# Optimization experiments

Hardware: AMD Instinct MI355X
Metric: run time of the kernel (lower is better)

Reference implementation:

```python
import jax, jax.numpy as jnp
import numpy as np
from jax import lax


def _bilinear_gather(img, ys, xs):
    """img: [B,H,W,C]; ys,xs: [B,K,H,W] fractional coords. Zero padding outside.
    Returns [B,K,H,W,C]."""
    B, H, W, C = img.shape
    y0 = jnp.floor(ys)
    x0 = jnp.floor(xs)
    wy = (ys - y0)[..., None]
    wx = (xs - x0)[..., None]
    y0i = y0.astype(jnp.int32)
    x0i = x0.astype(jnp.int32)
    flat = img.reshape(B, H * W, C)

    def gather(yi, xi):
        valid = (yi >= 0) & (yi < H) & (xi >= 0) & (xi < W)
        yc = jnp.clip(yi, 0, H - 1)
        xc = jnp.clip(xi, 0, W - 1)
        idx = (yc * W + xc).reshape(B, -1, 1)
        g = jnp.take_along_axis(flat, idx, axis=1).reshape(yi.shape + (C,))
        return g * valid[..., None].astype(img.dtype)

    v00 = gather(y0i, x0i)
    v01 = gather(y0i, x0i + 1)
    v10 = gather(y0i + 1, x0i)
    v11 = gather(y0i + 1, x0i + 1)
    one = jnp.asarray(1.0, img.dtype)
    return (v00 * (one - wy) * (one - wx) + v01 * (one - wy) * wx
            + v10 * wy * (one - wx) + v11 * wy * wx)


def _forward(x, w_off, b_off, w_def, b_def, w_attn, b_attn):
    B, Cin, H, W = x.shape
    Cout = w_def.shape[0]
    # offset conv: 3x3, pad 1 -> [B, 18, H, W]
    off = lax.conv_general_dilated(x, w_off, (1, 1), ((1, 1), (1, 1)))
    off = off + b_off[None, :, None, None]
    off = off.reshape(B, 9, 2, H, W)
    dy = off[:, :, 0]  # [B,9,H,W], torchvision order: (dy, dx) per kernel pt
    dx = off[:, :, 1]
    # kernel point grid, row-major over (kh, kw)
    ky, kx = jnp.meshgrid(jnp.arange(3), jnp.arange(3), indexing='ij')
    ky = ky.reshape(9).astype(x.dtype)
    kx = kx.reshape(9).astype(x.dtype)
    ii = jnp.arange(H, dtype=x.dtype)
    jj = jnp.arange(W, dtype=x.dtype)
    # sample position = (out_pos - pad + k) + offset, pad=1, stride=1
    ys = ii[None, None, :, None] - 1.0 + ky[None, :, None, None] + dy
    xs = jj[None, None, None, :] - 1.0 + kx[None, :, None, None] + dx
    img = x.transpose(0, 2, 3, 1)  # [B,H,W,Cin]
    sampled = _bilinear_gather(img, ys, xs)  # [B,9,H,W,Cin]
    wk = w_def.reshape(Cout, Cin, 9)  # row-major kernel pts match ky/kx
    out = jnp.einsum('bkhwc,ock->bohw', sampled, wk) + b_def[None, :, None, None]
    # spatial attention: 1x1 conv -> sigmoid gate
    attn = jnp.einsum('bchw,oc->bohw', out, w_attn[:, :, 0, 0]) + b_attn[None, :, None, None]
    out = out * jax.nn.sigmoid(attn)
    return jax.nn.relu(out)


def setup_inputs() -> dict:
    key = jax.random.key(0)
    ks = jax.random.split(key, 5)
    B, C, H, W = 4, 128, 128, 128
    x = jax.random.normal(ks[0], (B, C, H, W), dtype=jnp.float32)
    w_off = jax.random.normal(ks[1], (18, C, 3, 3), dtype=jnp.float32) * 0.02
    b_off = jnp.zeros((18,), dtype=jnp.float32)
    w_def = jax.random.normal(ks[2], (C, C, 3, 3), dtype=jnp.float32) * (1.0 / np.sqrt(C * 9))
    b_def = jnp.zeros((C,), dtype=jnp.float32)
    w_attn = jax.random.normal(ks[3], (1, C, 1, 1), dtype=jnp.float32) * (1.0 / np.sqrt(C))
    b_attn = jnp.zeros((1,), dtype=jnp.float32)
    return {"x": x, "w_off": w_off, "b_off": b_off, "w_def": w_def,
            "b_def": b_def, "w_attn": w_attn, "b_attn": b_attn}


def reference(x, w_off, b_off, w_def, b_def, w_attn, b_attn):
    return _forward(x, w_off, b_off, w_def, b_def, w_attn, b_attn)
```

## Files before the change

kernel.cpp:

```cpp
#include <hip/hip_runtime.h>
#include <math.h>

#define Cch 128
#define Hh 128
#define Ww 128
#define HW (Hh * Ww)

typedef __attribute__((ext_vector_type(8))) short short8;
typedef __attribute__((ext_vector_type(4))) float float4v;
typedef __attribute__((ext_vector_type(2))) float float2v;
typedef __attribute__((ext_vector_type(4))) unsigned int uint4v;

__device__ __forceinline__ unsigned short f2bf(float f) {
    unsigned u = __float_as_uint(f);
    return (unsigned short)((u + 0x8000u) >> 16);
}
__device__ __forceinline__ float2v up2(unsigned u) {
    return (float2v){__uint_as_float(u << 16), __uint_as_float(u & 0xffff0000u)};
}
__device__ __forceinline__ unsigned packbf2(float lo, float hi) {
    unsigned a = __float_as_uint(lo), b = __float_as_uint(hi);
    return ((a + 0x8000u) >> 16) | ((b + 0x8000u) & 0xffff0000u);
}

__global__ __launch_bounds__(256) void transpose_x_bf16(const float* __restrict__ x,
                                                        unsigned short* __restrict__ xt) {
    __shared__ float tile[32][33];
    int b  = blockIdx.z;
    int c0 = blockIdx.y * 32;
    int p0 = blockIdx.x * 32;
    int tx = threadIdx.x, ty = threadIdx.y;
    const float* xb = x + (size_t)b * Cch * HW;
    unsigned short* xtb = xt + (size_t)b * HW * Cch;
    #pragma unroll
    for (int i = 0; i < 32; i += 8)
        tile[ty + i][tx] = xb[(size_t)(c0 + ty + i) * HW + p0 + tx];
    __syncthreads();
    #pragma unroll
    for (int i = 0; i < 32; i += 8)
        xtb[(size_t)(p0 + ty + i) * Cch + c0 + tx] = f2bf(tile[tx][ty + i]);
}

#define NFB (9 * 4 * 8 * 64 * 8)
#define NFO (9 * 4 * 2 * 64 * 8)
__global__ __launch_bounds__(256) void build_frags(const float* __restrict__ w_def,
                                                   const float* __restrict__ w_off,
                                                   unsigned short* __restrict__ wfB,
                                                   unsigned short* __restrict__ wfO) {
    int idx = blockIdx.x * 256 + threadIdx.x;
    if (idx < NFB) {
        int j = idx & 7, lane = (idx >> 3) & 63, t = (idx >> 9) & 7;
        int q = (idx >> 12) & 3, k = idx >> 14;
        int c = 32 * q + 8 * (lane >> 4) + j;
        int o = 16 * t + (lane & 15);
        wfB[idx] = f2bf(w_def[(size_t)(o * Cch + c) * 9 + k]);
    } else if (idx < NFB + NFO) {
        int i2 = idx - NFB;
        int j = i2 & 7, lane = (i2 >> 3) & 63, t = (i2 >> 9) & 1;
        int q = (i2 >> 10) & 3, k = i2 >> 12;
        int c = 32 * q + 8 * (lane >> 4) + j;
        int o = 16 * t + (lane & 15);
        wfO[i2] = (o < 18) ? f2bf(w_off[(size_t)(o * Cch + c) * 9 + k]) : (unsigned short)0;
    }
}

__device__ __forceinline__ void blk_map(int blk, int& b, int& h, int& w0) {
    int xcd = blk & 7;
    b = xcd >> 1;
    int seg = ((xcd & 1) << 8) | (blk >> 3);
    h  = seg >> 2;
    w0 = (seg & 3) << 5;
}

__global__ __launch_bounds__(128, 2) void fused_srt(const unsigned short* __restrict__ xt,
                                                    const unsigned short* __restrict__ wfB,
                                                    const unsigned short* __restrict__ wfO,
                                                    const float* __restrict__ b_off,
                                                    const float* __restrict__ b_def,
                                                    const float* __restrict__ w_attn,
                                                    const float* __restrict__ b_attn,
                                                    float* __restrict__ out) {
    __shared__ float4v red[2 * 8 * 64];
    __shared__ float   offs[32 * 18];
    __shared__ uint4v  smw[2 * 4 * 64];
    int b, h, w0;
    blk_map(blockIdx.x, b, h, w0);
    int tid  = threadIdx.x;
    int wave = tid >> 6;
    int lane = tid & 63;
    int col  = lane & 15;
    int s    = lane >> 4;
    int spx  = lane >> 2;
    int sch  = lane & 3;
    int cbase = 64 * wave;
    int csrt  = cbase + sch * 8;
    int wbase = wave * 256;
    int rIdx  = wbase + ((lane & 15) * 4 + (lane >> 4));

    const unsigned short* xtb = xt + (size_t)b * HW * Cch;

    {
        float4v acc2[2][2];
        #pragma unroll
        for (int pt = 0; pt < 2; ++pt)
            #pragma unroll
            for (int t = 0; t < 2; ++t) {
                int o = 16 * t + col;
                float bv = (wave == 0 && o < 18) ? b_off[o] : 0.0f;
                acc2[pt][t] = (float4v){bv, bv, bv, bv};
            }

        #pragma unroll
        for (int k = 0; k < 9; ++k) {
            int y = h + (k / 3) - 1;
            bool vy = (y >= 0) && (y < Hh);
            int yc = min(max(y, 0), Hh - 1);
            int dxk = (k % 3) - 1;
            int  ofs[2];
            bool val[2];
            #pragma unroll
            for (int pt = 0; pt < 2; ++pt) {
                int px = w0 + 16 * pt + spx;
                int xs = px + dxk;
                val[pt] = vy && (xs >= 0) && (xs < Ww);
                int xc  = min(max(xs, 0), Ww - 1);
                ofs[pt] = (yc * Ww + xc) * Cch + csrt;
            }
            #pragma unroll
            for (int pt = 0; pt < 2; ++pt)
                #pragma unroll
                for (int qq = 0; qq < 2; ++qq) {
                    uint4v av = *(const uint4v*)(xtb + ofs[pt] + 32 * qq);
                    if (!val[pt]) av = (uint4v){0u, 0u, 0u, 0u};
                    smw[wbase + (pt * 2 + qq) * 64 + lane] = av;
                }
            short8 aa[2][2];
            #pragma unroll
            for (int pt = 0; pt < 2; ++pt)
                #pragma unroll
                for (int qq = 0; qq < 2; ++qq)
                    aa[pt][qq] = __builtin_bit_cast(short8, smw[rIdx + (pt * 2 + qq) * 64]);
            #pragma unroll
            for (int qq = 0; qq < 2; ++qq) {
                int q = 2 * wave + qq;
                #pragma unroll
                for (int t = 0; t < 2; ++t) {
                    short8 bv = *(const short8*)(wfO + ((size_t)((k * 4 + q) * 2 + t) * 64 + lane) * 8);
                    #pragma unroll
                    for (int pt = 0; pt < 2; ++pt)
                        acc2[pt][t] = __builtin_amdgcn_mfma_f32_16x16x32_bf16(aa[pt][qq], bv, acc2[pt][t], 0, 0, 0);
                }
            }
        }
        if (wave == 1) {
            #pragma unroll
            for (int pt = 0; pt < 2; ++pt)
                #pragma unroll
                for (int t = 0; t < 2; ++t)
                    red[(pt * 2 + t) * 64 + lane] = acc2[pt][t];
        }
        __syncthreads();
        if (wave == 0) {
            #pragma unroll
            for (int pt = 0; pt < 2; ++pt)
                #pragma unroll
                for (int t = 0; t < 2; ++t) {
                    float4v v = acc2[pt][t] + red[(pt * 2 + t) * 64 + lane];
                    int o = 16 * t + col;
                    if (o < 18) {
                        #pragma unroll
                        for (int r = 0; r < 4; ++r)
                            offs[(16 * pt + 4 * s + r) * 18 + o] = v[r];
                    }
                }
        }
        __syncthreads();
    }

    float4v acc[2][8];
    #pragma unroll
    for (int pt = 0; pt < 2; ++pt)
        #pragma unroll
        for (int t = 0; t < 8; ++t) {
            float bv = (wave == 0) ? b_def[16 * t + col] : 0.0f;
            acc[pt][t] = (float4v){bv, bv, bv, bv};
        }

    int    oaddr[2][4];
    float  wxy[2][4];
    uint4v u[2][8];

#define CALC_TAP(K_) do {                                                    \
    int ky = ((K_) * 11) >> 5;                                               \
    int kx = (K_) - 3 * ky;                                                  \
    _Pragma("unroll")                                                        \
    for (int pt = 0; pt < 2; ++pt) {                                         \
        int pxl = 16 * pt + spx;                                             \
        int px  = w0 + pxl;                                                  \
        float2 dv = *(const float2*)&offs[pxl * 18 + 2 * (K_)];              \
        float ys = (float)(h - 1 + ky) + dv.x;                               \
        float xs = (float)(px - 1 + kx) + dv.y;                              \
        float y0f = floorf(ys), x0f = floorf(xs);                            \
        float wy = ys - y0f, wx = xs - x0f;                                  \
        int y0 = (int)y0f, x0 = (int)x0f;                                    \
        bool vy0 = (y0 >= 0) && (y0 < Hh);                                   \
        bool vy1 = (y0 + 1 >= 0) && (y0 + 1 < Hh);                           \
        bool vx0 = (x0 >= 0) && (x0 < Ww);                                   \
        bool vx1 = (x0 + 1 >= 0) && (x0 + 1 < Ww);                           \
        int y0c = min(max(y0, 0), Hh - 1), y1c = min(max(y0 + 1, 0), Hh - 1);\
        int x0c = min(max(x0, 0), Ww - 1), x1c = min(max(x0 + 1, 0), Ww - 1);\
        wxy[pt][0] = vx0 ? (1.0f - wx) : 0.0f;                               \
        wxy[pt][1] = vx1 ? wx : 0.0f;                                        \
        wxy[pt][2] = vy0 ? (1.0f - wy) : 0.0f;                               \
        wxy[pt][3] = vy1 ? wy : 0.0f;                                        \
        oaddr[pt][0] = (y0c * Ww + x0c) * Cch + csrt;                        \
        oaddr[pt][1] = (y0c * Ww + x1c) * Cch + csrt;                        \
        oaddr[pt][2] = (y1c * Ww + x0c) * Cch + csrt;                        \
        oaddr[pt][3] = (y1c * Ww + x1c) * Cch + csrt;                        \
    }                                                                        \
} while (0)

#define LOAD_TAP() do {                                                      \
    _Pragma("unroll")                                                        \
    for (int pt = 0; pt < 2; ++pt)                                           \
        _Pragma("unroll")                                                    \
        for (int qq = 0; qq < 2; ++qq)                                       \
            _Pragma("unroll")                                                \
            for (int c4 = 0; c4 < 4; ++c4)                                   \
                u[pt][qq * 4 + c4] =                                         \
                    *(const uint4v*)(xtb + oaddr[pt][c4] + 32 * qq);         \
} while (0)

    CALC_TAP(0);
    LOAD_TAP();

    #pragma unroll
    for (int k = 0; k < 9; ++k) {
        const unsigned short* wk = wfB + (size_t)k * 16384 + (size_t)(2 * wave) * 4096;
        short8 bva[8], bvb[8];
        #pragma unroll
        for (int t = 0; t < 8; ++t) {
            bva[t] = *(const short8*)(wk + (size_t)t * 512 + (size_t)lane * 8);
            bvb[t] = *(const short8*)(wk + 4096 + (size_t)t * 512 + (size_t)lane * 8);
        }
        #pragma unroll
        for (int pt = 0; pt < 2; ++pt) {
            float2v A0 = (float2v){wxy[pt][0], wxy[pt][0]};
            float2v A1 = (float2v){wxy[pt][1], wxy[pt][1]};
            float2v B0 = (float2v){wxy[pt][2], wxy[pt][2]};
            float2v B1 = (float2v){wxy[pt][3], wxy[pt][3]};
            #pragma unroll
            for (int qq = 0; qq < 2; ++qq) {
                uint4v res;
                #pragma unroll
                for (int j = 0; j < 4; ++j) {
                    float2v p00 = up2(u[pt][qq * 4 + 0][j]);
                    float2v p01 = up2(u[pt][qq * 4 + 1][j]);
                    float2v p10 = up2(u[pt][qq * 4 + 2][j]);
                    float2v p11 = up2(u[pt][qq * 4 + 3][j]);
                    float2v t0 = __builtin_elementwise_fma(A1, p01, A0 * p00);
                    float2v t1 = __builtin_elementwise_fma(A1, p11, A0 * p10);
                    float2v rr = __builtin_elementwise_fma(B1, t1, B0 * t0);
                    res[j] = packbf2(rr.x, rr.y);
                }
                smw[wbase + (pt * 2 + qq) * 64 + lane] = res;
            }
        }
        if (k < 8) {
            CALC_TAP(k + 1);
            LOAD_TAP();
        }
        short8 afr[2][2];
        #pragma unroll
        for (int pt = 0; pt < 2; ++pt)
            #pragma unroll
            for (int qq = 0; qq < 2; ++qq)
                afr[pt][qq] = __builtin_bit_cast(short8, smw[rIdx + (pt * 2 + qq) * 64]);
        #pragma unroll
        for (int t = 0; t < 8; ++t) {
            acc[0][t] = __builtin_amdgcn_mfma_f32_16x16x32_bf16(afr[0][0], bva[t], acc[0][t], 0, 0, 0);
            acc[1][t] = __builtin_amdgcn_mfma_f32_16x16x32_bf16(afr[1][0], bva[t], acc[1][t], 0, 0, 0);
        }
        #pragma unroll
        for (int t = 0; t < 8; ++t) {
            acc[0][t] = __builtin_amdgcn_mfma_f32_16x16x32_bf16(afr[0][1], bvb[t], acc[0][t], 0, 0, 0);
            acc[1][t] = __builtin_amdgcn_mfma_f32_16x16x32_bf16(afr[1][1], bvb[t], acc[1][t], 0, 0, 0);
        }
    }
#undef CALC_TAP
#undef LOAD_TAP

    if (wave == 1) {
        #pragma unroll
        for (int pt = 0; pt < 2; ++pt)
            #pragma unroll
            for (int t = 0; t < 8; ++t)
                red[(pt * 8 + t) * 64 + lane] = acc[pt][t];
    }
    __syncthreads();
    if (wave == 0) {
        #pragma unroll
        for (int pt = 0; pt < 2; ++pt)
            #pragma unroll
            for (int t = 0; t < 8; ++t)
                acc[pt][t] += red[(pt * 8 + t) * 64 + lane];

        float wA[8];
        #pragma unroll
        for (int t = 0; t < 8; ++t) wA[t] = w_attn[16 * t + col];
        float battn = b_attn[0];
        #pragma unroll
        for (int pt = 0; pt < 2; ++pt) {
            float sig[4];
            #pragma unroll
            for (int r = 0; r < 4; ++r) {
                float pr = 0.0f;
                #pragma unroll
                for (int t = 0; t < 8; ++t) pr = fmaf(acc[pt][t][r], wA[t], pr);
                #pragma unroll
                for (int m = 1; m < 16; m <<= 1) pr += __shfl_xor(pr, m, 64);
                sig[r] = 1.0f / (1.0f + expf(-(pr + battn)));
            }
            #pragma unroll
            for (int t = 0; t < 8; ++t) {
                int o = 16 * t + col;
                #pragma unroll
                for (int r = 0; r < 4; ++r) {
                    int px = w0 + 16 * pt + 4 * s + r;
                    float v = acc[pt][t][r] * sig[r];
                    out[((size_t)(b * Cch + o)) * HW + h * Ww + px] = fmaxf(v, 0.0f);
                }
            }
        }
    }
}

extern "C" void kernel_launch(void* const* d_in, const int* in_sizes, int n_in,
                              void* d_out, int out_size, void* d_ws, size_t ws_size,
                              hipStream_t stream) {
    const float* x      = (const float*)d_in[0];
    const float* w_off  = (const float*)d_in[1];
    const float* b_off  = (const float*)d_in[2];
    const float* w_def  = (const float*)d_in[3];
    const float* b_def  = (const float*)d_in[4];
    const float* w_attn = (const float*)d_in[5];
    const float* b_attn = (const float*)d_in[6];
    float* out = (float*)d_out;

    char* ws = (char*)d_ws;
    unsigned short* xt  = (unsigned short*)ws;
    unsigned short* wfB = (unsigned short*)(ws + 16777216);
    unsigned short* wfO = (unsigned short*)(ws + 17072128);

    transpose_x_bf16<<<dim3(512, 4, 4), dim3(32, 8), 0, stream>>>(x, xt);
    build_frags<<<720, 256, 0, stream>>>(w_def, w_off, wfB, wfO);
    fused_srt<<<2048, 128, 0, stream>>>(xt, wfB, wfO, b_off, b_def, w_attn, b_attn, out);
}
```

Baseline: 153.5 us.

## Split input-channel reduction across four waves per block instead of two

The fused kernel now runs 4 waves per block, each owning 32 input channels rather than 64, which halves per-wave register use for gathered corners and weight fragments. The cross-wave sum is done as a two-level tree reduction through shared memory, at the cost of an extra barrier and more shared memory traffic. The separate address and load macros are merged so the next tap's gathers are issued directly, and launch bounds move to 256 threads with 3 blocks per CU to raise occupancy. More blocks resident per CU may raise cache pressure, and each wave has less independent work to hide latency.

```diff
diff --git a/kernel.cpp b/kernel.cpp
--- a/kernel.cpp
+++ b/kernel.cpp
@@ -72,17 +72,17 @@
     w0 = (seg & 3) << 5;
 }
 
-__global__ __launch_bounds__(128, 2) void fused_srt(const unsigned short* __restrict__ xt,
-                                                    const unsigned short* __restrict__ wfB,
-                                                    const unsigned short* __restrict__ wfO,
-                                                    const float* __restrict__ b_off,
-                                                    const float* __restrict__ b_def,
-                                                    const float* __restrict__ w_attn,
-                                                    const float* __restrict__ b_attn,
-                                                    float* __restrict__ out) {
-    __shared__ float4v red[2 * 8 * 64];
+__global__ __launch_bounds__(256, 3) void fused_q4(const unsigned short* __restrict__ xt,
+                                                   const unsigned short* __restrict__ wfB,
+                                                   const unsigned short* __restrict__ wfO,
+                                                   const float* __restrict__ b_off,
+                                                   const float* __restrict__ b_def,
+                                                   const float* __restrict__ w_attn,
+                                                   const float* __restrict__ b_attn,
+                                                   float* __restrict__ out) {
+    __shared__ float4v red[2048];
     __shared__ float   offs[32 * 18];
-    __shared__ uint4v  smw[2 * 4 * 64];
+    __shared__ uint4v  smw[4 * 2 * 64];
     int b, h, w0;
     blk_map(blockIdx.x, b, h, w0);
     int tid  = threadIdx.x;
@@ -92,10 +92,9 @@
     int s    = lane >> 4;
     int spx  = lane >> 2;
     int sch  = lane & 3;
-    int cbase = 64 * wave;
-    int csrt  = cbase + sch * 8;
-    int wbase = wave * 256;
-    int rIdx  = wbase + ((lane & 15) * 4 + (lane >> 4));
+    int csrt = 32 * wave + sch * 8;
+    int wbase = wave * 128;
+    int rr    = (lane & 15) * 4 + (lane >> 4);
 
     const unsigned short* xtb = xt + (size_t)b * HW * Cch;
 
@@ -116,40 +115,26 @@
             bool vy = (y >= 0) && (y < Hh);
             int yc = min(max(y, 0), Hh - 1);
             int dxk = (k % 3) - 1;
-            int  ofs[2];
-            bool val[2];
             #pragma unroll
             for (int pt = 0; pt < 2; ++pt) {
                 int px = w0 + 16 * pt + spx;
                 int xs = px + dxk;
-                val[pt] = vy && (xs >= 0) && (xs < Ww);
+                bool val = vy && (xs >= 0) && (xs < Ww);
                 int xc  = min(max(xs, 0), Ww - 1);
-                ofs[pt] = (yc * Ww + xc) * Cch + csrt;
-            }
-            #pragma unroll
-            for (int pt = 0; pt < 2; ++pt)
-                #pragma unroll
-                for (int qq = 0; qq < 2; ++qq) {
-                    uint4v av = *(const uint4v*)(xtb + ofs[pt] + 32 * qq);
-                    if (!val[pt]) av = (uint4v){0u, 0u, 0u, 0u};
-                    smw[wbase + (pt * 2 + qq) * 64 + lane] = av;
-                }
-            short8 aa[2][2];
-            #pragma unroll
-            for (int pt = 0; pt < 2; ++pt)
-                #pragma unroll
-                for (int qq = 0; qq < 2; ++qq)
-                    aa[pt][qq] = __builtin_bit_cast(short8, smw[rIdx + (pt * 2 + qq) * 64]);
-            #pragma unroll
-            for (int qq = 0; qq < 2; ++qq) {
-                int q = 2 * wave + qq;
-                #pragma unroll
-                for (int t = 0; t < 2; ++t) {
-                    short8 bv = *(const short8*)(wfO + ((size_t)((k * 4 + q) * 2 + t) * 64 + lane) * 8);
-                    #pragma unroll
-                    for (int pt = 0; pt < 2; ++pt)
-                        acc2[pt][t] = __builtin_amdgcn_mfma_f32_16x16x32_bf16(aa[pt][qq], bv, acc2[pt][t], 0, 0, 0);
-                }
+                uint4v av = *(const uint4v*)(xtb + (yc * Ww + xc) * Cch + csrt);
+                if (!val) av = (uint4v){0u, 0u, 0u, 0u};
+                smw[wbase + pt * 64 + lane] = av;
+            }
+            short8 aa[2];
+            #pragma unroll
+            for (int pt = 0; pt < 2; ++pt)
+                aa[pt] = __builtin_bit_cast(short8, smw[wbase + pt * 64 + rr]);
+            #pragma unroll
+            for (int t = 0; t < 2; ++t) {
+                short8 bv = *(const short8*)(wfO + ((size_t)((k * 4 + wave) * 2 + t) * 64 + lane) * 8);
+                #pragma unroll
+                for (int pt = 0; pt < 2; ++pt)
+                    acc2[pt][t] = __builtin_amdgcn_mfma_f32_16x16x32_bf16(aa[pt], bv, acc2[pt][t], 0, 0, 0);
             }
         }
         if (wave == 1) {
@@ -159,13 +144,37 @@
                 for (int t = 0; t < 2; ++t)
                     red[(pt * 2 + t) * 64 + lane] = acc2[pt][t];
         }
+        if (wave == 3) {
+            #pragma unroll
+            for (int pt = 0; pt < 2; ++pt)
+                #pragma unroll
+                for (int t = 0; t < 2; ++t)
+                    red[1024 + (pt * 2 + t) * 64 + lane] = acc2[pt][t];
+        }
         __syncthreads();
         if (wave == 0) {
             #pragma unroll
             for (int pt = 0; pt < 2; ++pt)
                 #pragma unroll
+                for (int t = 0; t < 2; ++t)
+                    acc2[pt][t] += red[(pt * 2 + t) * 64 + lane];
+        }
+        if (wave == 2) {
+            #pragma unroll
+            for (int pt = 0; pt < 2; ++pt)
+                #pragma unroll
                 for (int t = 0; t < 2; ++t) {
-                    float4v v = acc2[pt][t] + red[(pt * 2 + t) * 64 + lane];
+                    acc2[pt][t] += red[1024 + (pt * 2 + t) * 64 + lane];
+                    red[1024 + (pt * 2 + t) * 64 + lane] = acc2[pt][t];
+                }
+        }
+        __syncthreads();
+        if (wave == 0) {
+            #pragma unroll
+            for (int pt = 0; pt < 2; ++pt)
+                #pragma unroll
+                for (int t = 0; t < 2; ++t) {
+                    float4v v = acc2[pt][t] + red[1024 + (pt * 2 + t) * 64 + lane];
                     int o = 16 * t + col;
                     if (o < 18) {
                         #pragma unroll
@@ -186,11 +195,10 @@
             acc[pt][t] = (float4v){bv, bv, bv, bv};
         }
 
-    int    oaddr[2][4];
     float  wxy[2][4];
-    uint4v u[2][8];
-
-#define CALC_TAP(K_) do {                                                    \
+    uint4v u[2][4];
+
+#define CALC_LOAD_TAP(K_) do {                                               \
     int ky = ((K_) * 11) >> 5;                                               \
     int kx = (K_) - 3 * ky;                                                  \
     _Pragma("unroll")                                                        \
@@ -213,82 +221,54 @@
         wxy[pt][1] = vx1 ? wx : 0.0f;                                        \
         wxy[pt][2] = vy0 ? (1.0f - wy) : 0.0f;                               \
         wxy[pt][3] = vy1 ? wy : 0.0f;                                        \
-        oaddr[pt][0] = (y0c * Ww + x0c) * Cch + csrt;                        \
-        oaddr[pt][1] = (y0c * Ww + x1c) * Cch + csrt;                        \
-        oaddr[pt][2] = (y1c * Ww + x0c) * Cch + csrt;                        \
-        oaddr[pt][3] = (y1c * Ww + x1c) * Cch + csrt;                        \
+        u[pt][0] = *(const uint4v*)(xtb + (y0c * Ww + x0c) * Cch + csrt);    \
+        u[pt][1] = *(const uint4v*)(xtb + (y0c * Ww + x1c) * Cch + csrt);    \
+        u[pt][2] = *(const uint4v*)(xtb + (y1c * Ww + x0c) * Cch + csrt);    \
+        u[pt][3] = *(const uint4v*)(xtb + (y1c * Ww + x1c) * Cch + csrt);    \
     }                                                                        \
 } while (0)
 
-#define LOAD_TAP() do {                                                      \
-    _Pragma("unroll")                                                        \
-    for (int pt = 0; pt < 2; ++pt)                                           \
-        _Pragma("unroll")                                                    \
-        for (int qq = 0; qq < 2; ++qq)                                       \
-            _Pragma("unroll")                                                \
-            for (int c4 = 0; c4 < 4; ++c4)                                   \
-                u[pt][qq * 4 + c4] =                                         \
-                    *(const uint4v*)(xtb + oaddr[pt][c4] + 32 * qq);         \
-} while (0)
-
-    CALC_TAP(0);
-    LOAD_TAP();
+    CALC_LOAD_TAP(0);
 
     #pragma unroll
     for (int k = 0; k < 9; ++k) {
-        const unsigned short* wk = wfB + (size_t)k * 16384 + (size_t)(2 * wave) * 4096;
-        short8 bva[8], bvb[8];
-        #pragma unroll
-        for (int t = 0; t < 8; ++t) {
-            bva[t] = *(const short8*)(wk + (size_t)t * 512 + (size_t)lane * 8);
-            bvb[t] = *(const short8*)(wk + 4096 + (size_t)t * 512 + (size_t)lane * 8);
-        }
         #pragma unroll
         for (int pt = 0; pt < 2; ++pt) {
             float2v A0 = (float2v){wxy[pt][0], wxy[pt][0]};
             float2v A1 = (float2v){wxy[pt][1], wxy[pt][1]};
             float2v B0 = (float2v){wxy[pt][2], wxy[pt][2]};
             float2v B1 = (float2v){wxy[pt][3], wxy[pt][3]};
-            #pragma unroll
-            for (int qq = 0; qq < 2; ++qq) {
-                uint4v res;
-                #pragma unroll
-                for (int j = 0; j < 4; ++j) {
-                    float2v p00 = up2(u[pt][qq * 4 + 0][j]);
-                    float2v p01 = up2(u[pt][qq * 4 + 1][j]);
-                    float2v p10 = up2(u[pt][qq * 4 + 2][j]);
-                    float2v p11 = up2(u[pt][qq * 4 + 3][j]);
-                    float2v t0 = __builtin_elementwise_fma(A1, p01, A0 * p00);
-                    float2v t1 = __builtin_elementwise_fma(A1, p11, A0 * p10);
-                    float2v rr = __builtin_elementwise_fma(B1, t1, B0 * t0);
-                    res[j] = packbf2(rr.x, rr.y);
-                }
-                smw[wbase + (pt * 2 + qq) * 64 + lane] = res;
-            }
-        }
-        if (k < 8) {
-            CALC_TAP(k + 1);
-            LOAD_TAP();
-        }
-        short8 afr[2][2];
-        #pragma unroll
-        for (int pt = 0; pt < 2; ++pt)
-            #pragma unroll
-            for (int qq = 0; qq < 2; ++qq)
-                afr[pt][qq] = __builtin_bit_cast(short8, smw[rIdx + (pt * 2 + qq) * 64]);
+            uint4v res;
+            #pragma unroll
+            for (int j = 0; j < 4; ++j) {
+                float2v p00 = up2(u[pt][0][j]);
+                float2v p01 = up2(u[pt][1][j]);
+                float2v p10 = up2(u[pt][2][j]);
+                float2v p11 = up2(u[pt][3][j]);
+                float2v t0 = __builtin_elementwise_fma(A1, p01, A0 * p00);
+                float2v t1 = __builtin_elementwise_fma(A1, p11, A0 * p10);
+                float2v rr2 = __builtin_elementwise_fma(B1, t1, B0 * t0);
+                res[j] = packbf2(rr2.x, rr2.y);
+            }
+            smw[wbase + pt * 64 + lane] = res;
+        }
+        const unsigned short* wk = wfB + (size_t)(k * 4 + wave) * 4096;
+        short8 bw[8];
+        #pragma unroll
+        for (int t = 0; t < 8; ++t)
+            bw[t] = *(const short8*)(wk + (size_t)t * 512 + (size_t)lane * 8);
+        if (k < 8) CALC_LOAD_TAP(k + 1);
+        short8 afr[2];
+        #pragma unroll
+        for (int pt = 0; pt < 2; ++pt)
+            afr[pt] = __builtin_bit_cast(short8, smw[wbase + pt * 64 + rr]);
         #pragma unroll
         for (int t = 0; t < 8; ++t) {
-            acc[0][t] = __builtin_amdgcn_mfma_f32_16x16x32_bf16(afr[0][0], bva[t], acc[0][t], 0, 0, 0);
-            acc[1][t] = __builtin_amdgcn_mfma_f32_16x16x32_bf16(afr[1][0], bva[t], acc[1][t], 0, 0, 0);
-        }
-        #pragma unroll
-        for (int t = 0; t < 8; ++t) {
-            acc[0][t] = __builtin_amdgcn_mfma_f32_16x16x32_bf16(afr[0][1], bvb[t], acc[0][t], 0, 0, 0);
-            acc[1][t] = __builtin_amdgcn_mfma_f32_16x16x32_bf16(afr[1][1], bvb[t], acc[1][t], 0, 0, 0);
-        }
-    }
-#undef CALC_TAP
-#undef LOAD_TAP
+            acc[0][t] = __builtin_amdgcn_mfma_f32_16x16x32_bf16(afr[0], bw[t], acc[0][t], 0, 0, 0);
+            acc[1][t] = __builtin_amdgcn_mfma_f32_16x16x32_bf16(afr[1], bw[t], acc[1][t], 0, 0, 0);
+        }
+    }
+#undef CALC_LOAD_TAP
 
     if (wave == 1) {
         #pragma unroll
@@ -297,6 +277,13 @@
             for (int t = 0; t < 8; ++t)
                 red[(pt * 8 + t) * 64 + lane] = acc[pt][t];
     }
+    if (wave == 3) {
+        #pragma unroll
+        for (int pt = 0; pt < 2; ++pt)
+            #pragma unroll
+            for (int t = 0; t < 8; ++t)
+                red[1024 + (pt * 8 + t) * 64 + lane] = acc[pt][t];
+    }
     __syncthreads();
     if (wave == 0) {
         #pragma unroll
@@ -304,6 +291,23 @@
             #pragma unroll
             for (int t = 0; t < 8; ++t)
                 acc[pt][t] += red[(pt * 8 + t) * 64 + lane];
+    }
+    if (wave == 2) {
+        #pragma unroll
+        for (int pt = 0; pt < 2; ++pt)
+            #pragma unroll
+            for (int t = 0; t < 8; ++t) {
+                acc[pt][t] += red[1024 + (pt * 8 + t) * 64 + lane];
+                red[1024 + (pt * 8 + t) * 64 + lane] = acc[pt][t];
+            }
+    }
+    __syncthreads();
+    if (wave == 0) {
+        #pragma unroll
+        for (int pt = 0; pt < 2; ++pt)
+            #pragma unroll
+            for (int t = 0; t < 8; ++t)
+                acc[pt][t] += red[1024 + (pt * 8 + t) * 64 + lane];
 
         float wA[8];
         #pragma unroll
@@ -354,5 +358,5 @@
 
     transpose_x_bf16<<<dim3(512, 4, 4), dim3(32, 8), 0, stream>>>(x, xt);
     build_frags<<<720, 256, 0, stream>>>(w_def, w_off, wfB, wfO);
-    fused_srt<<<2048, 128, 0, stream>>>(xt, wfB, wfO, b_off, b_def, w_attn, b_attn, out);
-}
+    fused_q4<<<2048, 256, 0, stream>>>(xt, wfB, wfO, b_off, b_def, w_attn, b_attn, out);
+}
```

Result: slower. 196.2 us (+27.8%).
